# Kernel tuning notes

Hardware: AMD Instinct MI355X
Metric: run time of the kernel (lower is better)

The kernel has to match this reference:

```python
import jax, jax.numpy as jnp
import numpy as np

BATCH, L, D_OUT, D_HID = 8, 8192, 512, 256
R_MIN, R_MAX, MAX_PHASE = 0.9, 0.999, 6.28


def setup_inputs() -> dict:
    key = jax.random.key(0)
    ks = jax.random.split(key, 10)
    x = jax.random.normal(ks[0], (BATCH, L, D_OUT), jnp.float32)
    # input_dense (nn.Dense(d_out)) params
    W = jax.random.normal(ks[1], (D_OUT, D_OUT), jnp.float32) / jnp.sqrt(jnp.float32(D_OUT))
    b = jnp.zeros((D_OUT,), jnp.float32)
    # nu_log / theta_log per the flax initializers
    u1 = jax.random.uniform(ks[2], (D_HID,), jnp.float32)
    nu_log = jnp.log(-0.5 * jnp.log(u1 * (R_MAX**2 - R_MIN**2) + R_MIN**2))
    u2 = jax.random.uniform(ks[3], (D_HID,), jnp.float32)
    theta_log = jnp.log(MAX_PHASE * u2)
    diag_lambda = jnp.exp(-jnp.exp(nu_log) + 1j * jnp.exp(theta_log))
    gamma_log = jnp.log(jnp.sqrt(1.0 - jnp.abs(diag_lambda) ** 2))
    B_re = jax.random.normal(ks[4], (D_HID, D_OUT), jnp.float32) / jnp.sqrt(jnp.float32(2 * D_OUT))
    B_im = jax.random.normal(ks[5], (D_HID, D_OUT), jnp.float32) / jnp.sqrt(jnp.float32(2 * D_OUT))
    C_re = jax.random.normal(ks[6], (D_OUT, D_HID), jnp.float32) / jnp.sqrt(jnp.float32(D_HID))
    C_im = jax.random.normal(ks[7], (D_OUT, D_HID), jnp.float32) / jnp.sqrt(jnp.float32(D_HID))
    D = jax.random.normal(ks[8], (D_OUT,), jnp.float32)
    return {"x": x, "W": W, "b": b, "nu_log": nu_log, "theta_log": theta_log,
            "gamma_log": gamma_log, "B_re": B_re, "B_im": B_im,
            "C_re": C_re, "C_im": C_im, "D": D}


def _binop(q_i, q_j):
    # associative op for diagonal linear recurrence h_t = A_t h_{t-1} + b_t
    A_i, b_i = q_i
    A_j, b_j = q_j
    return (A_j * A_i, A_j * b_i + b_j)


def reference(x, W, b, nu_log, theta_log, gamma_log, B_re, B_im, C_re, C_im, D):
    xp = x @ W + b                                            # [B,L,d_out]
    lam = jnp.exp(-jnp.exp(nu_log) + 1j * jnp.exp(theta_log))  # [N] complex
    B_norm = (B_re + 1j * B_im) * jnp.exp(gamma_log)[:, None]  # [N,d_out]
    Bu = xp.astype(B_norm.dtype) @ B_norm.T                    # [B,L,N] complex
    Lam = jnp.broadcast_to(lam, Bu.shape)
    # parallel scan over sequence axis (axis=1); elementwise binop, batch broadcasts
    _, h = jax.lax.associative_scan(_binop, (Lam, Bu), axis=1)  # [B,L,N]
    C = C_re + 1j * C_im                                        # [d_out,N]
    outputs = jnp.real(h @ C.T) + D * xp                        # [B,L,d_out]
    return outputs, h[:, -1]
```

## Files before the change

### kernel.cpp

```cpp
#include <hip/hip_runtime.h>
#include <hip/hip_bf16.h>
#include <math.h>

#define BATCH   8
#define SEQL    8192
#define DOUTD   512
#define DHID    256
#define MTOT    (BATCH*SEQL)
#define CHUNKS  128
#define CHUNKLN 64
#define SQUAR   6

typedef __bf16 bh;
typedef __bf16 bh8 __attribute__((ext_vector_type(8)));
typedef float  f32x4 __attribute__((ext_vector_type(4)));

__global__ void conv_x_kernel(const float4* __restrict__ x, bh* __restrict__ xh) {
    long i = (long)blockIdx.x * 256 + threadIdx.x;
    float4 a = x[2 * i], c = x[2 * i + 1];
    bh8 o;
    o[0] = (bh)a.x; o[1] = (bh)a.y; o[2] = (bh)a.z; o[3] = (bh)a.w;
    o[4] = (bh)c.x; o[5] = (bh)c.y; o[6] = (bh)c.z; o[7] = (bh)c.w;
    *(bh8*)(xh + i * 8) = o;
}

__global__ void prep0_kernel(const float* __restrict__ nu_log, const float* __restrict__ theta_log,
                             const float* __restrict__ gamma_log, const float* __restrict__ Bre,
                             const float* __restrict__ Bim, const float* __restrict__ bvec,
                             const float* __restrict__ Dvec,
                             float* lamRe, float* lamIm, float* lamSRe, float* lamSIm,
                             float* gamma, float* bB, float* bD) {
    int t = threadIdx.x;
    if (t < 512) bD[t] = bvec[t] * Dvec[t];
    if (t < 256) {
        float nu = expf(nu_log[t]);
        float th = expf(theta_log[t]);
        float mag = expf(-nu);
        float lr = mag * cosf(th), li = mag * sinf(th);
        lamRe[t] = lr; lamIm[t] = li;
        float pr = lr, pi = li;
        for (int s = 0; s < SQUAR; ++s) { float nr = pr*pr - pi*pi, ni = 2.f*pr*pi; pr = nr; pi = ni; }
        lamSRe[t] = pr; lamSIm[t] = pi;
        float g = expf(gamma_log[t]);
        gamma[t] = g;
        float sre = 0.f, sim = 0.f;
        for (int k = 0; k < 512; ++k) {
            float bk = bvec[k];
            sre += bk * Bre[t * 512 + k];
            sim += bk * Bim[t * 512 + k];
        }
        bB[t] = sre * g; bB[t + 256] = sim * g;
    }
}

__global__ void transposeW_kernel(const float* __restrict__ W, float* __restrict__ Wt) {
    __shared__ float t[64][65];
    const int bx = blockIdx.x & 7, by = blockIdx.x >> 3;
    const int r0 = by * 64, c0 = bx * 64;
    const int tr = threadIdx.x >> 4;
    const int tc = (threadIdx.x & 15) * 4;
#pragma unroll
    for (int rr = 0; rr < 64; rr += 16) {
        float4 v = *(const float4*)&W[(size_t)(r0 + tr + rr) * 512 + c0 + tc];
        t[tr + rr][tc + 0] = v.x; t[tr + rr][tc + 1] = v.y;
        t[tr + rr][tc + 2] = v.z; t[tr + rr][tc + 3] = v.w;
    }
    __syncthreads();
#pragma unroll
    for (int rr = 0; rr < 64; rr += 16) {
        const int orow = tr + rr;
        float4 o;
        o.x = t[tc + 0][orow]; o.y = t[tc + 1][orow];
        o.z = t[tc + 2][orow]; o.w = t[tc + 3][orow];
        *(float4*)&Wt[(size_t)(c0 + orow) * 512 + r0 + tc] = o;
    }
}

__global__ void prepWB_kernel(const float* __restrict__ Wt, const float* __restrict__ Bre,
                              const float* __restrict__ Bim, const float* __restrict__ gamma,
                              bh* __restrict__ WBt) {
    __shared__ float bsh[4][512];
    const int c0 = blockIdx.x * 4;
    const int tid = threadIdx.x;
    for (int i = tid; i < 2048; i += 256) {
        int ci = i >> 9, k = i & 511;
        int c = c0 + ci;
        float v = (c < 256) ? Bre[(size_t)c * 512 + k] : Bim[(size_t)(c - 256) * 512 + k];
        bsh[ci][k] = v * gamma[c & 255];
    }
    __syncthreads();
    const int j = tid * 2;
    float a0[4] = {}, a1[4] = {};
    for (int k = 0; k < 512; ++k) {
        float2 wv = *(const float2*)&Wt[(size_t)k * 512 + j];
#pragma unroll
        for (int ci = 0; ci < 4; ++ci) {
            float b = bsh[ci][k];
            a0[ci] += wv.x * b;
            a1[ci] += wv.y * b;
        }
    }
#pragma unroll
    for (int ci = 0; ci < 4; ++ci) {
        WBt[(size_t)(c0 + ci) * 512 + j]     = (bh)a0[ci];
        WBt[(size_t)(c0 + ci) * 512 + j + 1] = (bh)a1[ci];
    }
}

__global__ void prepWC_kernel(const float* __restrict__ Cre, const float* __restrict__ Cim,
                              const float* __restrict__ Wt, const float* __restrict__ Dvec,
                              bh* __restrict__ WcT) {
    int e = blockIdx.x * 256 + threadIdx.x;
    int c = e >> 10, kp = e & 1023;
    float v;
    if (kp < 256)       v = Cre[c * 256 + kp];
    else if (kp < 512)  v = -Cim[c * 256 + (kp - 256)];
    else                v = Wt[(size_t)c * 512 + (kp - 512)] * Dvec[c];
    WcT[e] = (bh)v;
}


#define MMAQ(mh, nh) \
  _Pragma("unroll") for (int ks = 0; ks < 2; ++ks) \
  _Pragma("unroll") for (int mi = 0; mi < 4; ++mi) \
  _Pragma("unroll") for (int ni = 0; ni < 2; ++ni) \
    acc[(mh)*4+mi][(nh)*2+ni] = __builtin_amdgcn_mfma_f32_16x16x32_bf16( \
        afr[mi*2+ks], bfr[ni*2+ks], acc[(mh)*4+mi][(nh)*2+ni], 0, 0, 0);

#define PH_MMA(mh, nh) \
  __builtin_amdgcn_s_barrier(); \
  __builtin_amdgcn_s_setprio(1); \
  MMAQ(mh, nh) \
  __builtin_amdgcn_s_setprio(0); \
  __builtin_amdgcn_s_barrier();

template<int KTOT, bool SPLIT_A, bool OUT_F32>
__global__ __launch_bounds__(512, 2)
void gemm_kernel(const bh* __restrict__ A0, const bh* __restrict__ A1,
                 const bh* __restrict__ Bw, const float* __restrict__ bias,
                 float* __restrict__ outF, bh* __restrict__ outH) {
    __shared__ alignas(16) bh lds[65536];
    const int tid = threadIdx.x;
    const int l = tid & 63, w = tid >> 6;
    const int wm = w >> 2, wn = w & 3;
    const int bid = blockIdx.x, nwg = gridDim.x;
    const int swz = (bid & 7) * (nwg >> 3) + (bid >> 3);
    const int rowBase = (swz >> 1) * 256;
    const int colBase = (swz & 1) * 256;
    const int rsub = l & 15, g = l >> 4;
    const int r7 = rsub & 7;
    const int sl0 = ((0 + g) ^ r7) * 8;
    const int sl1 = ((4 + g) ^ r7) * 8;
    const int st_r  = tid >> 3;
    const int st_sl = ((tid & 7) ^ (st_r & 7)) * 8;
    const int st_ld = (tid & 7) * 8;

    f32x4 acc[8][4] = {};
    bh8 afr[8];
    bh8 bfr[4];

    const int NT  = KTOT / 64;
    const int NIT = NT / 2;

    auto stageA = [&](int t, int half, int bufsel) {
        const int k0 = t * 64;
        const bh* As = A0; int kk = k0;
        if (SPLIT_A && k0 >= 512) { As = A1; kk = k0 - 512; }
        bh* lb = &lds[bufsel * 32768];
#pragma unroll
        for (int j = 0; j < 2; ++j) {
            const int rt = half * 128 + j * 64 + st_r;
            const bh* ga = As + (size_t)(rowBase + rt) * 512 + kk + st_sl;
            __builtin_amdgcn_global_load_lds(
                (const __attribute__((address_space(1))) void*)ga,
                (__attribute__((address_space(3))) void*)&lb[rt * 64 + st_ld], 16, 0, 0);
        }
    };
    auto stageB = [&](int t, int half, int bufsel) {
        const int k0 = t * 64;
        bh* lb = &lds[bufsel * 32768 + 16384];
#pragma unroll
        for (int j = 0; j < 2; ++j) {
            const int rt = half * 128 + j * 64 + st_r;
            const bh* gb = Bw + (size_t)(colBase + rt) * KTOT + k0 + st_sl;
            __builtin_amdgcn_global_load_lds(
                (const __attribute__((address_space(1))) void*)gb,
                (__attribute__((address_space(3))) void*)&lb[rt * 64 + st_ld], 16, 0, 0);
        }
    };
    auto dsA = [&](int mh, int bufsel) {
        const bh* lb = &lds[bufsel * 32768];
#pragma unroll
        for (int mi = 0; mi < 4; ++mi) {
            const int row = wm * 128 + (mh * 4 + mi) * 16 + rsub;
            afr[mi * 2 + 0] = *(const bh8*)&lb[row * 64 + sl0];
            afr[mi * 2 + 1] = *(const bh8*)&lb[row * 64 + sl1];
        }
    };
    auto dsB = [&](int nh, int bufsel) {
        const bh* lb = &lds[bufsel * 32768 + 16384];
#pragma unroll
        for (int ni = 0; ni < 2; ++ni) {
            const int row = wn * 64 + (nh * 2 + ni) * 16 + rsub;
            bfr[ni * 2 + 0] = *(const bh8*)&lb[row * 64 + sl0];
            bfr[ni * 2 + 1] = *(const bh8*)&lb[row * 64 + sl1];
        }
    };

    stageA(0, 0, 0); stageA(0, 1, 0); stageB(0, 0, 0); stageB(0, 1, 0);
    stageA(1, 0, 1);
    asm volatile("s_waitcnt vmcnt(2)" ::: "memory");
    __builtin_amdgcn_sched_barrier(0);
    __builtin_amdgcn_s_barrier();

    for (int i = 0; i < NIT; ++i) {
        const int t0 = 2 * i, t1 = 2 * i + 1;
        dsA(0, 0); dsB(0, 0);
        stageA(t1, 1, 1);
        PH_MMA(0, 0)
        dsB(1, 0);
        stageB(t1, 0, 1);
        PH_MMA(0, 1)
        dsA(1, 0);
        stageB(t1, 1, 1);
        PH_MMA(1, 1)
        dsB(0, 0);
        if (t0 + 2 < NT) stageA(t0 + 2, 0, 0);
        __builtin_amdgcn_s_barrier();
        __builtin_amdgcn_s_setprio(1);
        MMAQ(1, 0)
        __builtin_amdgcn_s_setprio(0);
        if (t0 + 2 < NT) { asm volatile("s_waitcnt vmcnt(2)" ::: "memory"); }
        else             { asm volatile("s_waitcnt vmcnt(0)" ::: "memory"); }
        __builtin_amdgcn_sched_barrier(0);
        __builtin_amdgcn_s_barrier();
        dsA(0, 1); dsB(0, 1);
        if (t0 + 2 < NT) stageA(t0 + 2, 1, 0);
        PH_MMA(0, 0)
        dsB(1, 1);
        if (t0 + 2 < NT) stageB(t0 + 2, 0, 0);
        PH_MMA(0, 1)
        dsA(1, 1);
        if (t0 + 2 < NT) stageB(t0 + 2, 1, 0);
        PH_MMA(1, 1)
        dsB(0, 1);
        if (t1 + 2 < NT) stageA(t1 + 2, 0, 1);
        __builtin_amdgcn_s_barrier();
        __builtin_amdgcn_s_setprio(1);
        MMAQ(1, 0)
        __builtin_amdgcn_s_setprio(0);
        if (t1 + 2 < NT) { asm volatile("s_waitcnt vmcnt(2)" ::: "memory"); }
        else             { asm volatile("s_waitcnt vmcnt(0)" ::: "memory"); }
        __builtin_amdgcn_sched_barrier(0);
        __builtin_amdgcn_s_barrier();
    }

#pragma unroll
    for (int m = 0; m < 8; ++m)
#pragma unroll
        for (int j = 0; j < 4; ++j) {
            const int row = rowBase + wm * 128 + m * 16 + g * 4 + j;
#pragma unroll
            for (int n = 0; n < 4; ++n) {
                const int col = colBase + wn * 64 + n * 16 + rsub;
                float v = acc[m][n][j] + bias[col];
                if (OUT_F32) outF[(size_t)row * 512 + col] = v;
                else         outH[(size_t)row * 512 + col] = (bh)v;
            }
        }
}

__global__ void scan1_kernel(const bh* __restrict__ Bu, const float* __restrict__ lamRe,
                             const float* __restrict__ lamIm, float* __restrict__ carRe,
                             float* __restrict__ carIm) {
    int b = blockIdx.x >> 7, c = blockIdx.x & (CHUNKS - 1);
    int n = threadIdx.x;
    float lr = lamRe[n], li = lamIm[n];
    float hr = 0.f, hi = 0.f;
    const bh* p = Bu + ((size_t)(b * SEQL + c * CHUNKLN)) * 512;
    for (int i = 0; i < CHUNKLN; ++i) {
        float br = (float)p[n], bi = (float)p[n + 256];
        float nr = lr * hr - li * hi + br;
        float ni = lr * hi + li * hr + bi;
        hr = nr; hi = ni; p += 512;
    }
    carRe[(size_t)blockIdx.x * 256 + n] = hr;
    carIm[(size_t)blockIdx.x * 256 + n] = hi;
}

__global__ void scan2_kernel(const float* __restrict__ carRe, const float* __restrict__ carIm,
                             const float* __restrict__ lamSRe, const float* __restrict__ lamSIm,
                             float* __restrict__ iniRe, float* __restrict__ iniIm) {
    int b = blockIdx.x, n = threadIdx.x;
    float lr = lamSRe[n], li = lamSIm[n];
    float hr = 0.f, hi = 0.f;
    for (int c = 0; c < CHUNKS; ++c) {
        size_t idx = ((size_t)b * CHUNKS + c) * 256 + n;
        iniRe[idx] = hr; iniIm[idx] = hi;
        float cr = carRe[idx], ci = carIm[idx];
        float nr = lr * hr - li * hi + cr;
        float ni = lr * hi + li * hr + ci;
        hr = nr; hi = ni;
    }
}

__global__ void scan3_kernel(bh* __restrict__ Bu, const float* __restrict__ lamRe,
                             const float* __restrict__ lamIm, const float* __restrict__ iniRe,
                             const float* __restrict__ iniIm, float* __restrict__ outTail,
                             int tailN) {
    int b = blockIdx.x >> 7, c = blockIdx.x & (CHUNKS - 1);
    int n = threadIdx.x;
    float lr = lamRe[n], li = lamIm[n];
    size_t idx = (size_t)blockIdx.x * 256 + n;
    float hr = iniRe[idx], hi = iniIm[idx];
    bh* p = Bu + ((size_t)(b * SEQL + c * CHUNKLN)) * 512;
    for (int i = 0; i < CHUNKLN; ++i) {
        float br = (float)p[n], bi = (float)p[n + 256];
        float nr = lr * hr - li * hi + br;
        float ni = lr * hi + li * hr + bi;
        hr = nr; hi = ni;
        p[n] = (bh)hr; p[n + 256] = (bh)hi;
        p += 512;
    }
    if (c == CHUNKS - 1) {
        if (tailN >= 4096) {
            outTail[b * 256 + n]        = hr;
            outTail[2048 + b * 256 + n] = hi;
        } else {
            outTail[b * 256 + n] = hr;
        }
    }
}

extern "C" void kernel_launch(void* const* d_in, const int* in_sizes, int n_in,
                              void* d_out, int out_size, void* d_ws, size_t ws_size,
                              hipStream_t stream) {
    const float* x        = (const float*)d_in[0];
    const float* W        = (const float*)d_in[1];
    const float* bvec     = (const float*)d_in[2];
    const float* nu_log   = (const float*)d_in[3];
    const float* theta_lg = (const float*)d_in[4];
    const float* gamma_lg = (const float*)d_in[5];
    const float* Bre      = (const float*)d_in[6];
    const float* Bim      = (const float*)d_in[7];
    const float* Cre      = (const float*)d_in[8];
    const float* Cim      = (const float*)d_in[9];
    const float* Dvec     = (const float*)d_in[10];

    char* ws = (char*)d_ws;
    bh* xh   = (bh*)(ws);
    bh* bu   = (bh*)(ws + 67108864);
    bh* wbt  = (bh*)(ws + 134217728);
    bh* wct  = (bh*)(ws + 134217728 + 524288);
    float* Wt = (float*)(ws + 134217728 + 524288 + 1048576);
    float* sm = (float*)(ws + 134217728 + 524288 + 1048576 + 1048576);
    float* bB = sm;
    float* bD = sm + 512;
    float* lamRe  = sm + 1024;
    float* lamIm  = sm + 1280;
    float* lamSRe = sm + 1536;
    float* lamSIm = sm + 1792;
    float* gamma  = sm + 2048;
    float* carRe  = sm + 2304;
    float* carIm  = carRe + (size_t)BATCH * CHUNKS * 256;
    float* iniRe  = carIm + (size_t)BATCH * CHUNKS * 256;
    float* iniIm  = iniRe + (size_t)BATCH * CHUNKS * 256;

    float* outF    = (float*)d_out;
    float* outTail = outF + (size_t)MTOT * DOUTD;
    int tailN = out_size - MTOT * DOUTD;

    conv_x_kernel<<<16384, 256, 0, stream>>>((const float4*)x, xh);
    prep0_kernel<<<1, 512, 0, stream>>>(nu_log, theta_lg, gamma_lg, Bre, Bim, bvec, Dvec,
                                        lamRe, lamIm, lamSRe, lamSIm, gamma, bB, bD);
    transposeW_kernel<<<64, 256, 0, stream>>>(W, Wt);
    prepWB_kernel<<<128, 256, 0, stream>>>(Wt, Bre, Bim, gamma, wbt);
    prepWC_kernel<<<2048, 256, 0, stream>>>(Cre, Cim, Wt, Dvec, wct);

    gemm_kernel<512, false, false><<<512, 512, 0, stream>>>(xh, nullptr, wbt, bB, nullptr, bu);

    scan1_kernel<<<BATCH * CHUNKS, 256, 0, stream>>>(bu, lamRe, lamIm, carRe, carIm);
    scan2_kernel<<<BATCH, 256, 0, stream>>>(carRe, carIm, lamSRe, lamSIm, iniRe, iniIm);
    scan3_kernel<<<BATCH * CHUNKS, 256, 0, stream>>>(bu, lamRe, lamIm, iniRe, iniIm, outTail, tailN);

    gemm_kernel<1024, true, true><<<512, 512, 0, stream>>>(bu, xh, wct, bD, outF, nullptr);
}
```

Measured before the change: 291.3 us.

## Fuse fp32-to-bf16 conversion of x into first GEMM and merge prep kernels

The first GEMM now loads x directly in fp32 through registers, converts it to bf16 while writing it into LDS, and also writes the bf16 copy that the second GEMM needs (only from blocks with colBase 0). This removes the standalone conversion kernel's separate full read and write pass over x. The parameter-prep kernel is folded into the W-transpose launch as an extra block, which saves one launch. The cost is that A-tile loads go through registers instead of direct-to-LDS loads, which adds register pressure and conversion work inside the GEMM main loop. Column-half-1 blocks also read x in fp32 a second time.

```diff
diff --git a/kernel.cpp b/kernel.cpp
--- a/kernel.cpp
+++ b/kernel.cpp
@@ -15,45 +15,38 @@
 typedef __bf16 bh8 __attribute__((ext_vector_type(8)));
 typedef float  f32x4 __attribute__((ext_vector_type(4)));
 
-__global__ void conv_x_kernel(const float4* __restrict__ x, bh* __restrict__ xh) {
-    long i = (long)blockIdx.x * 256 + threadIdx.x;
-    float4 a = x[2 * i], c = x[2 * i + 1];
-    bh8 o;
-    o[0] = (bh)a.x; o[1] = (bh)a.y; o[2] = (bh)a.z; o[3] = (bh)a.w;
-    o[4] = (bh)c.x; o[5] = (bh)c.y; o[6] = (bh)c.z; o[7] = (bh)c.w;
-    *(bh8*)(xh + i * 8) = o;
-}
-
-__global__ void prep0_kernel(const float* __restrict__ nu_log, const float* __restrict__ theta_log,
-                             const float* __restrict__ gamma_log, const float* __restrict__ Bre,
-                             const float* __restrict__ Bim, const float* __restrict__ bvec,
-                             const float* __restrict__ Dvec,
-                             float* lamRe, float* lamIm, float* lamSRe, float* lamSIm,
-                             float* gamma, float* bB, float* bD) {
-    int t = threadIdx.x;
-    if (t < 512) bD[t] = bvec[t] * Dvec[t];
-    if (t < 256) {
-        float nu = expf(nu_log[t]);
-        float th = expf(theta_log[t]);
-        float mag = expf(-nu);
-        float lr = mag * cosf(th), li = mag * sinf(th);
-        lamRe[t] = lr; lamIm[t] = li;
-        float pr = lr, pi = li;
-        for (int s = 0; s < SQUAR; ++s) { float nr = pr*pr - pi*pi, ni = 2.f*pr*pi; pr = nr; pi = ni; }
-        lamSRe[t] = pr; lamSIm[t] = pi;
-        float g = expf(gamma_log[t]);
-        gamma[t] = g;
-        float sre = 0.f, sim = 0.f;
-        for (int k = 0; k < 512; ++k) {
-            float bk = bvec[k];
-            sre += bk * Bre[t * 512 + k];
-            sim += bk * Bim[t * 512 + k];
-        }
-        bB[t] = sre * g; bB[t + 256] = sim * g;
-    }
-}
-
-__global__ void transposeW_kernel(const float* __restrict__ W, float* __restrict__ Wt) {
+__global__ void transposeW_kernel(const float* __restrict__ W, float* __restrict__ Wt,
+                                  const float* __restrict__ nu_log, const float* __restrict__ theta_log,
+                                  const float* __restrict__ gamma_log, const float* __restrict__ Bre,
+                                  const float* __restrict__ Bim, const float* __restrict__ bvec,
+                                  const float* __restrict__ Dvec,
+                                  float* lamRe, float* lamIm, float* lamSRe, float* lamSIm,
+                                  float* gamma, float* bB, float* bD) {
+    if (blockIdx.x == 64) {
+        int tid = threadIdx.x;
+        for (int t = tid; t < 512; t += 256) bD[t] = bvec[t] * Dvec[t];
+        int t = tid;
+        if (t < 256) {
+            float nu = expf(nu_log[t]);
+            float th = expf(theta_log[t]);
+            float mag = expf(-nu);
+            float lr = mag * cosf(th), li = mag * sinf(th);
+            lamRe[t] = lr; lamIm[t] = li;
+            float pr = lr, pi = li;
+            for (int s = 0; s < SQUAR; ++s) { float nr = pr*pr - pi*pi, ni = 2.f*pr*pi; pr = nr; pi = ni; }
+            lamSRe[t] = pr; lamSIm[t] = pi;
+            float g = expf(gamma_log[t]);
+            gamma[t] = g;
+            float sre = 0.f, sim = 0.f;
+            for (int k = 0; k < 512; ++k) {
+                float bk = bvec[k];
+                sre += bk * Bre[t * 512 + k];
+                sim += bk * Bim[t * 512 + k];
+            }
+            bB[t] = sre * g; bB[t + 256] = sim * g;
+        }
+        return;
+    }
     __shared__ float t[64][65];
     const int bx = blockIdx.x & 7, by = blockIdx.x >> 3;
     const int r0 = by * 64, c0 = bx * 64;
@@ -119,7 +112,6 @@
     WcT[e] = (bh)v;
 }
 
-
 #define MMAQ(mh, nh) \
   _Pragma("unroll") for (int ks = 0; ks < 2; ++ks) \
   _Pragma("unroll") for (int mi = 0; mi < 4; ++mi) \
@@ -133,6 +125,142 @@
   MMAQ(mh, nh) \
   __builtin_amdgcn_s_setprio(0); \
   __builtin_amdgcn_s_barrier();
+
+__global__ __launch_bounds__(512, 2)
+void gemmA_kernel(const float* __restrict__ X, const bh* __restrict__ Bw,
+                  const float* __restrict__ bias, bh* __restrict__ outH,
+                  bh* __restrict__ xh) {
+    __shared__ alignas(16) bh lds[65536];
+    const int tid = threadIdx.x;
+    const int l = tid & 63, w = tid >> 6;
+    const int wm = w >> 2, wn = w & 3;
+    const int bid = blockIdx.x, nwg = gridDim.x;
+    const int swz = (bid & 7) * (nwg >> 3) + (bid >> 3);
+    const int rowBase = (swz >> 1) * 256;
+    const int colBase = (swz & 1) * 256;
+    const int rsub = l & 15, g = l >> 4;
+    const int r7 = rsub & 7;
+    const int sl0 = ((0 + g) ^ r7) * 8;
+    const int sl1 = ((4 + g) ^ r7) * 8;
+    const int st_r  = tid >> 3;
+    const int st_sl = ((tid & 7) ^ (st_r & 7)) * 8;
+    const int st_ld = (tid & 7) * 8;
+    const int ar  = tid >> 1;
+    const int as0 = (tid & 1) * 4;
+
+    f32x4 acc[8][4] = {};
+    bh8 afr[8];
+    bh8 bfr[4];
+    float4 xa[8];
+
+    const int NT = 8, NIT = 4;
+
+    auto issueAx = [&](int t) {
+        const float* gp = X + (size_t)(rowBase + ar) * 512 + t * 64 + as0 * 8;
+#pragma unroll
+        for (int q = 0; q < 8; ++q) xa[q] = ((const float4*)gp)[q];
+        asm volatile("" ::: "memory");
+    };
+    auto writeAx = [&](int t, int bufsel) {
+        bh* lb = &lds[bufsel * 32768];
+#pragma unroll
+        for (int q = 0; q < 4; ++q) {
+            float4 a = xa[2 * q], b = xa[2 * q + 1];
+            bh8 v;
+            v[0] = (bh)a.x; v[1] = (bh)a.y; v[2] = (bh)a.z; v[3] = (bh)a.w;
+            v[4] = (bh)b.x; v[5] = (bh)b.y; v[6] = (bh)b.z; v[7] = (bh)b.w;
+            const int slot = (as0 + q) ^ (ar & 7);
+            *(bh8*)&lb[ar * 64 + slot * 8] = v;
+            if (colBase == 0)
+                *(bh8*)&xh[(size_t)(rowBase + ar) * 512 + t * 64 + (as0 + q) * 8] = v;
+        }
+        asm volatile("" ::: "memory");
+    };
+    auto stageB = [&](int t, int half, int bufsel) {
+        const int k0 = t * 64;
+        bh* lb = &lds[bufsel * 32768 + 16384];
+#pragma unroll
+        for (int j = 0; j < 2; ++j) {
+            const int rt = half * 128 + j * 64 + st_r;
+            const bh* gb = Bw + (size_t)(colBase + rt) * 512 + k0 + st_sl;
+            __builtin_amdgcn_global_load_lds(
+                (const __attribute__((address_space(1))) void*)gb,
+                (__attribute__((address_space(3))) void*)&lb[rt * 64 + st_ld], 16, 0, 0);
+        }
+    };
+    auto dsA = [&](int mh, int bufsel) {
+        const bh* lb = &lds[bufsel * 32768];
+#pragma unroll
+        for (int mi = 0; mi < 4; ++mi) {
+            const int row = wm * 128 + (mh * 4 + mi) * 16 + rsub;
+            afr[mi * 2 + 0] = *(const bh8*)&lb[row * 64 + sl0];
+            afr[mi * 2 + 1] = *(const bh8*)&lb[row * 64 + sl1];
+        }
+    };
+    auto dsB = [&](int nh, int bufsel) {
+        const bh* lb = &lds[bufsel * 32768 + 16384];
+#pragma unroll
+        for (int ni = 0; ni < 2; ++ni) {
+            const int row = wn * 64 + (nh * 2 + ni) * 16 + rsub;
+            bfr[ni * 2 + 0] = *(const bh8*)&lb[row * 64 + sl0];
+            bfr[ni * 2 + 1] = *(const bh8*)&lb[row * 64 + sl1];
+        }
+    };
+
+    issueAx(0);
+    stageB(0, 0, 0); stageB(0, 1, 0);
+    writeAx(0, 0);
+    asm volatile("s_waitcnt vmcnt(0) lgkmcnt(0)" ::: "memory");
+    __builtin_amdgcn_s_barrier();
+
+    for (int i = 0; i < NIT; ++i) {
+        const int t0 = 2 * i, t1 = 2 * i + 1;
+        dsA(0, 0); dsB(0, 0);
+        issueAx(t1);
+        PH_MMA(0, 0)
+        dsB(1, 0);
+        stageB(t1, 0, 1); stageB(t1, 1, 1);
+        PH_MMA(0, 1)
+        dsA(1, 0);
+        writeAx(t1, 1);
+        PH_MMA(1, 1)
+        dsB(0, 0);
+        __builtin_amdgcn_s_barrier();
+        __builtin_amdgcn_s_setprio(1);
+        MMAQ(1, 0)
+        __builtin_amdgcn_s_setprio(0);
+        asm volatile("s_waitcnt vmcnt(0) lgkmcnt(0)" ::: "memory");
+        __builtin_amdgcn_s_barrier();
+        dsA(0, 1); dsB(0, 1);
+        if (t0 + 2 < NT) issueAx(t0 + 2);
+        PH_MMA(0, 0)
+        dsB(1, 1);
+        if (t0 + 2 < NT) { stageB(t0 + 2, 0, 0); stageB(t0 + 2, 1, 0); }
+        PH_MMA(0, 1)
+        dsA(1, 1);
+        if (t0 + 2 < NT) writeAx(t0 + 2, 0);
+        PH_MMA(1, 1)
+        dsB(0, 1);
+        __builtin_amdgcn_s_barrier();
+        __builtin_amdgcn_s_setprio(1);
+        MMAQ(1, 0)
+        __builtin_amdgcn_s_setprio(0);
+        asm volatile("s_waitcnt vmcnt(0) lgkmcnt(0)" ::: "memory");
+        __builtin_amdgcn_s_barrier();
+    }
+
+#pragma unroll
+    for (int m = 0; m < 8; ++m)
+#pragma unroll
+        for (int j = 0; j < 4; ++j) {
+            const int row = rowBase + wm * 128 + m * 16 + g * 4 + j;
+#pragma unroll
+            for (int n = 0; n < 4; ++n) {
+                const int col = colBase + wn * 64 + n * 16 + rsub;
+                outH[(size_t)row * 512 + col] = (bh)(acc[m][n][j] + bias[col]);
+            }
+        }
+}
 
 template<int KTOT, bool SPLIT_A, bool OUT_F32>
 __global__ __launch_bounds__(512, 2)
@@ -370,14 +498,13 @@
     float* outTail = outF + (size_t)MTOT * DOUTD;
     int tailN = out_size - MTOT * DOUTD;
 
-    conv_x_kernel<<<16384, 256, 0, stream>>>((const float4*)x, xh);
-    prep0_kernel<<<1, 512, 0, stream>>>(nu_log, theta_lg, gamma_lg, Bre, Bim, bvec, Dvec,
-                                        lamRe, lamIm, lamSRe, lamSIm, gamma, bB, bD);
-    transposeW_kernel<<<64, 256, 0, stream>>>(W, Wt);
+    transposeW_kernel<<<65, 256, 0, stream>>>(W, Wt, nu_log, theta_lg, gamma_lg,
+                                              Bre, Bim, bvec, Dvec,
+                                              lamRe, lamIm, lamSRe, lamSIm, gamma, bB, bD);
     prepWB_kernel<<<128, 256, 0, stream>>>(Wt, Bre, Bim, gamma, wbt);
     prepWC_kernel<<<2048, 256, 0, stream>>>(Cre, Cim, Wt, Dvec, wct);
 
-    gemm_kernel<512, false, false><<<512, 512, 0, stream>>>(xh, nullptr, wbt, bB, nullptr, bu);
+    gemmA_kernel<<<512, 512, 0, stream>>>(x, wbt, bB, bu, xh);
 
     scan1_kernel<<<BATCH * CHUNKS, 256, 0, stream>>>(bu, lamRe, lamIm, carRe, carIm);
     scan2_kernel<<<BATCH, 256, 0, stream>>>(carRe, carIm, lamSRe, lamSIm, iniRe, iniIm);
```

After: 350.8 us. 20.4% more time.

## Interleave Re/Im columns of Bu and fuse setup kernels into two launches

Applied to the files above, without the earlier changes.

Reorders the WB weight rows and WC weight columns so the Bu/h buffer stores real and imaginary parts interleaved. Each scan thread can then load and store both halves as one 32-bit word instead of two strided 16-bit accesses. It also merges the five preprocessing kernels into two launches with blockIdx-based dispatch to cut launch overhead. The bias bB is reindexed to match, which adds coupling across the GEMM, scan and weight layouts.

```diff
diff --git a/kernel.cpp b/kernel.cpp
--- a/kernel.cpp
+++ b/kernel.cpp
@@ -13,25 +13,55 @@
 
 typedef __bf16 bh;
 typedef __bf16 bh8 __attribute__((ext_vector_type(8)));
+typedef __bf16 bh2 __attribute__((ext_vector_type(2)));
 typedef float  f32x4 __attribute__((ext_vector_type(4)));
 
-__global__ void conv_x_kernel(const float4* __restrict__ x, bh* __restrict__ xh) {
-    long i = (long)blockIdx.x * 256 + threadIdx.x;
-    float4 a = x[2 * i], c = x[2 * i + 1];
-    bh8 o;
-    o[0] = (bh)a.x; o[1] = (bh)a.y; o[2] = (bh)a.z; o[3] = (bh)a.w;
-    o[4] = (bh)c.x; o[5] = (bh)c.y; o[6] = (bh)c.z; o[7] = (bh)c.w;
-    *(bh8*)(xh + i * 8) = o;
-}
-
-__global__ void prep0_kernel(const float* __restrict__ nu_log, const float* __restrict__ theta_log,
+
+__global__ void setup_kernel(const float4* __restrict__ x, bh* __restrict__ xh,
+                             const float* __restrict__ W, float* __restrict__ Wt,
+                             const float* __restrict__ nu_log, const float* __restrict__ theta_log,
                              const float* __restrict__ gamma_log, const float* __restrict__ Bre,
                              const float* __restrict__ Bim, const float* __restrict__ bvec,
                              const float* __restrict__ Dvec,
                              float* lamRe, float* lamIm, float* lamSRe, float* lamSIm,
                              float* gamma, float* bB, float* bD) {
-    int t = threadIdx.x;
-    if (t < 512) bD[t] = bvec[t] * Dvec[t];
+    int bid = blockIdx.x;
+    if (bid < 16384) {
+        long i = (long)bid * 256 + threadIdx.x;
+        float4 a = x[2 * i], c = x[2 * i + 1];
+        bh8 o;
+        o[0] = (bh)a.x; o[1] = (bh)a.y; o[2] = (bh)a.z; o[3] = (bh)a.w;
+        o[4] = (bh)c.x; o[5] = (bh)c.y; o[6] = (bh)c.z; o[7] = (bh)c.w;
+        *(bh8*)(xh + i * 8) = o;
+        return;
+    }
+    bid -= 16384;
+    if (bid < 64) {
+        __shared__ float t[64][65];
+        const int bx = bid & 7, by = bid >> 3;
+        const int r0 = by * 64, c0 = bx * 64;
+        const int tr = threadIdx.x >> 4;
+        const int tc = (threadIdx.x & 15) * 4;
+#pragma unroll
+        for (int rr = 0; rr < 64; rr += 16) {
+            float4 v = *(const float4*)&W[(size_t)(r0 + tr + rr) * 512 + c0 + tc];
+            t[tr + rr][tc + 0] = v.x; t[tr + rr][tc + 1] = v.y;
+            t[tr + rr][tc + 2] = v.z; t[tr + rr][tc + 3] = v.w;
+        }
+        __syncthreads();
+#pragma unroll
+        for (int rr = 0; rr < 64; rr += 16) {
+            const int orow = tr + rr;
+            float4 o;
+            o.x = t[tc + 0][orow]; o.y = t[tc + 1][orow];
+            o.z = t[tc + 2][orow]; o.w = t[tc + 3][orow];
+            *(float4*)&Wt[(size_t)(c0 + orow) * 512 + r0 + tc] = o;
+        }
+        return;
+    }
+    int tid = threadIdx.x;
+    for (int t = tid; t < 512; t += 256) bD[t] = bvec[t] * Dvec[t];
+    int t = tid;
     if (t < 256) {
         float nu = expf(nu_log[t]);
         float th = expf(theta_log[t]);
@@ -49,76 +79,58 @@
             sre += bk * Bre[t * 512 + k];
             sim += bk * Bim[t * 512 + k];
         }
-        bB[t] = sre * g; bB[t + 256] = sim * g;
-    }
-}
-
-__global__ void transposeW_kernel(const float* __restrict__ W, float* __restrict__ Wt) {
-    __shared__ float t[64][65];
-    const int bx = blockIdx.x & 7, by = blockIdx.x >> 3;
-    const int r0 = by * 64, c0 = bx * 64;
-    const int tr = threadIdx.x >> 4;
-    const int tc = (threadIdx.x & 15) * 4;
-#pragma unroll
-    for (int rr = 0; rr < 64; rr += 16) {
-        float4 v = *(const float4*)&W[(size_t)(r0 + tr + rr) * 512 + c0 + tc];
-        t[tr + rr][tc + 0] = v.x; t[tr + rr][tc + 1] = v.y;
-        t[tr + rr][tc + 2] = v.z; t[tr + rr][tc + 3] = v.w;
-    }
-    __syncthreads();
-#pragma unroll
-    for (int rr = 0; rr < 64; rr += 16) {
-        const int orow = tr + rr;
-        float4 o;
-        o.x = t[tc + 0][orow]; o.y = t[tc + 1][orow];
-        o.z = t[tc + 2][orow]; o.w = t[tc + 3][orow];
-        *(float4*)&Wt[(size_t)(c0 + orow) * 512 + r0 + tc] = o;
-    }
-}
-
-__global__ void prepWB_kernel(const float* __restrict__ Wt, const float* __restrict__ Bre,
+        bB[2 * t]     = sre * g;
+        bB[2 * t + 1] = sim * g;
+    }
+}
+
+__global__ void prepBC_kernel(const float* __restrict__ Wt, const float* __restrict__ Bre,
                               const float* __restrict__ Bim, const float* __restrict__ gamma,
-                              bh* __restrict__ WBt) {
-    __shared__ float bsh[4][512];
-    const int c0 = blockIdx.x * 4;
-    const int tid = threadIdx.x;
-    for (int i = tid; i < 2048; i += 256) {
-        int ci = i >> 9, k = i & 511;
-        int c = c0 + ci;
-        float v = (c < 256) ? Bre[(size_t)c * 512 + k] : Bim[(size_t)(c - 256) * 512 + k];
-        bsh[ci][k] = v * gamma[c & 255];
-    }
-    __syncthreads();
-    const int j = tid * 2;
-    float a0[4] = {}, a1[4] = {};
-    for (int k = 0; k < 512; ++k) {
-        float2 wv = *(const float2*)&Wt[(size_t)k * 512 + j];
+                              bh* __restrict__ WBt,
+                              const float* __restrict__ Cre, const float* __restrict__ Cim,
+                              const float* __restrict__ Dvec, bh* __restrict__ WcT) {
+    if (blockIdx.x < 128) {
+        __shared__ float bsh[4][512];
+        const int c0 = blockIdx.x * 4;
+        const int tid = threadIdx.x;
+        for (int i = tid; i < 2048; i += 256) {
+            int ci = i >> 9, k = i & 511;
+            int c = c0 + ci;
+            float v = (c < 256) ? Bre[(size_t)c * 512 + k] : Bim[(size_t)(c - 256) * 512 + k];
+            bsh[ci][k] = v * gamma[c & 255];
+        }
+        __syncthreads();
+        const int j = tid * 2;
+        float a0[4] = {}, a1[4] = {};
+        for (int k = 0; k < 512; ++k) {
+            float2 wv = *(const float2*)&Wt[(size_t)k * 512 + j];
+#pragma unroll
+            for (int ci = 0; ci < 4; ++ci) {
+                float b = bsh[ci][k];
+                a0[ci] += wv.x * b;
+                a1[ci] += wv.y * b;
+            }
+        }
 #pragma unroll
         for (int ci = 0; ci < 4; ++ci) {
-            float b = bsh[ci][k];
-            a0[ci] += wv.x * b;
-            a1[ci] += wv.y * b;
-        }
-    }
-#pragma unroll
-    for (int ci = 0; ci < 4; ++ci) {
-        WBt[(size_t)(c0 + ci) * 512 + j]     = (bh)a0[ci];
-        WBt[(size_t)(c0 + ci) * 512 + j + 1] = (bh)a1[ci];
-    }
-}
-
-__global__ void prepWC_kernel(const float* __restrict__ Cre, const float* __restrict__ Cim,
-                              const float* __restrict__ Wt, const float* __restrict__ Dvec,
-                              bh* __restrict__ WcT) {
-    int e = blockIdx.x * 256 + threadIdx.x;
+            const int c = c0 + ci;
+            const int r = (c < 256) ? 2 * c : 2 * (c - 256) + 1;
+            WBt[(size_t)r * 512 + j]     = (bh)a0[ci];
+            WBt[(size_t)r * 512 + j + 1] = (bh)a1[ci];
+        }
+        return;
+    }
+    int e = (blockIdx.x - 128) * 256 + threadIdx.x;
     int c = e >> 10, kp = e & 1023;
     float v;
-    if (kp < 256)       v = Cre[c * 256 + kp];
-    else if (kp < 512)  v = -Cim[c * 256 + (kp - 256)];
-    else                v = Wt[(size_t)c * 512 + (kp - 512)] * Dvec[c];
+    if (kp < 512) {
+        int n = kp >> 1;
+        v = (kp & 1) ? -Cim[c * 256 + n] : Cre[c * 256 + n];
+    } else {
+        v = Wt[(size_t)c * 512 + (kp - 512)] * Dvec[c];
+    }
     WcT[e] = (bh)v;
 }
-
 
 #define MMAQ(mh, nh) \
   _Pragma("unroll") for (int ks = 0; ks < 2; ++ks) \
@@ -277,12 +289,14 @@
     int n = threadIdx.x;
     float lr = lamRe[n], li = lamIm[n];
     float hr = 0.f, hi = 0.f;
-    const bh* p = Bu + ((size_t)(b * SEQL + c * CHUNKLN)) * 512;
+    const unsigned* p = (const unsigned*)Bu + ((size_t)(b * SEQL + c * CHUNKLN)) * 256 + n;
     for (int i = 0; i < CHUNKLN; ++i) {
-        float br = (float)p[n], bi = (float)p[n + 256];
+        unsigned u = *p;
+        float br = __uint_as_float(u << 16);
+        float bi = __uint_as_float(u & 0xffff0000u);
         float nr = lr * hr - li * hi + br;
         float ni = lr * hi + li * hr + bi;
-        hr = nr; hi = ni; p += 512;
+        hr = nr; hi = ni; p += 256;
     }
     carRe[(size_t)blockIdx.x * 256 + n] = hr;
     carIm[(size_t)blockIdx.x * 256 + n] = hi;
@@ -313,14 +327,17 @@
     float lr = lamRe[n], li = lamIm[n];
     size_t idx = (size_t)blockIdx.x * 256 + n;
     float hr = iniRe[idx], hi = iniIm[idx];
-    bh* p = Bu + ((size_t)(b * SEQL + c * CHUNKLN)) * 512;
+    unsigned* p = (unsigned*)Bu + ((size_t)(b * SEQL + c * CHUNKLN)) * 256 + n;
     for (int i = 0; i < CHUNKLN; ++i) {
-        float br = (float)p[n], bi = (float)p[n + 256];
+        unsigned u = *p;
+        float br = __uint_as_float(u << 16);
+        float bi = __uint_as_float(u & 0xffff0000u);
         float nr = lr * hr - li * hi + br;
         float ni = lr * hi + li * hr + bi;
         hr = nr; hi = ni;
-        p[n] = (bh)hr; p[n + 256] = (bh)hi;
-        p += 512;
+        bh2 o; o[0] = (bh)hr; o[1] = (bh)hi;
+        *(bh2*)p = o;
+        p += 256;
     }
     if (c == CHUNKS - 1) {
         if (tailN >= 4096) {
@@ -370,12 +387,10 @@
     float* outTail = outF + (size_t)MTOT * DOUTD;
     int tailN = out_size - MTOT * DOUTD;
 
-    conv_x_kernel<<<16384, 256, 0, stream>>>((const float4*)x, xh);
-    prep0_kernel<<<1, 512, 0, stream>>>(nu_log, theta_lg, gamma_lg, Bre, Bim, bvec, Dvec,
-                                        lamRe, lamIm, lamSRe, lamSIm, gamma, bB, bD);
-    transposeW_kernel<<<64, 256, 0, stream>>>(W, Wt);
-    prepWB_kernel<<<128, 256, 0, stream>>>(Wt, Bre, Bim, gamma, wbt);
-    prepWC_kernel<<<2048, 256, 0, stream>>>(Cre, Cim, Wt, Dvec, wct);
+    setup_kernel<<<16449, 256, 0, stream>>>((const float4*)x, xh, W, Wt,
+                                            nu_log, theta_lg, gamma_lg, Bre, Bim, bvec, Dvec,
+                                            lamRe, lamIm, lamSRe, lamSIm, gamma, bB, bD);
+    prepBC_kernel<<<2176, 256, 0, stream>>>(Wt, Bre, Bim, gamma, wbt, Cre, Cim, Dvec, wct);
 
     gemm_kernel<512, false, false><<<512, 512, 0, stream>>>(xh, nullptr, wbt, bB, nullptr, bu);
 
```

New measurement: 282.4 us. 3.0% less time.
